# Performance work log

Measured on AMD Instinct MI355X. Metric: run time of the kernel, lower is better.

The kernel has to match this reference:

```python
import jax, jax.numpy as jnp
import numpy as np
from jax import lax

sg = lax.stop_gradient

# (kernel, stride, pad, pool_k, pool_s) for the 7 conv blocks
CFG = [(16, 2, 7, 8, 4), (12, 2, 5, 4, 2), (9, 1, 4, 5, 2), (7, 1, 3, 4, 2),
       (5, 1, 2, 2, 2), (3, 1, 1, 2, 2), (3, 1, 1, 2, 2)]
W_SHAPES = [(8, 1, 16), (12, 8, 12), (32, 12, 9), (64, 32, 7),
            (64, 64, 5), (64, 64, 3), (72, 64, 3)]
CH = [8, 12, 32, 64, 64, 64, 72]


def bin_act(x):
    # forward: sign(x); backward: clipped-quadratic surrogate (STE)
    s = jnp.sign(x)
    le = (x < -1.0).astype(x.dtype)
    ri = (x >= 1.0).astype(x.dtype)
    cl = ((x >= -1.0) & (x < 0.0)).astype(x.dtype)
    cr = ((x >= 0.0) & (x < 1.0)).astype(x.dtype)
    out = cl * (2.0 + x) * x + cr * (2.0 - x) * x + ri - le
    return sg(s) + out - sg(out)


def bin_wei(w, axes):
    # forward: scale * sign(w) with scale = mean|w| (detached); backward through tanh (STE)
    scale = sg(jnp.mean(jnp.abs(w), axis=axes, keepdims=True))
    t = jnp.tanh(w)
    return sg(scale * jnp.sign(w)) + t - sg(t)


def conv1d(x, w, stride, pad):
    return lax.conv_general_dilated(x, w, (stride,), [(pad, pad)],
                                    dimension_numbers=('NCH', 'OIH', 'NCH'))


def maxpool1d(x, k, s):
    return lax.reduce_window(x, -jnp.inf, lax.max, (1, 1, k), (1, 1, s), 'VALID')


def batchnorm1d(x, gamma, beta, eps=1e-5):
    # training-mode BN: batch statistics over (N, L), biased variance
    m = jnp.mean(x, axis=(0, 2), keepdims=True)
    v = jnp.mean((x - m) ** 2, axis=(0, 2), keepdims=True)
    return gamma[None, :, None] * (x - m) / jnp.sqrt(v + eps) + beta[None, :, None]


def _forward(x, ws, gs, bs, wfc):
    for w, g, b, (k, s, p, pk, ps) in zip(ws, gs, bs, CFG):
        x = conv1d(x, bin_wei(w, (1, 2)), s, p)
        x = maxpool1d(x, pk, ps)
        x = batchnorm1d(x, g, b)
        x = bin_act(x)
    x = x.reshape(x.shape[0], -1)                 # [B, 72*3]
    return x @ bin_wei(wfc, (1,)).T               # [B, classCount]


def setup_inputs() -> dict:
    key = jax.random.key(0)
    ks = jax.random.split(key, 9)
    inp = {'x': jax.random.normal(ks[0], (2048, 1, 3600), dtype=jnp.float32)}
    for i, shp in enumerate(W_SHAPES):
        inp[f'w{i+1}'] = jax.random.uniform(ks[i + 1], shp, dtype=jnp.float32) * 0.32
        inp[f'g{i+1}'] = jnp.ones((CH[i],), jnp.float32)
        inp[f'b{i+1}'] = jnp.zeros((CH[i],), jnp.float32)
    inp['wfc'] = jax.random.uniform(ks[8], (5, 216), dtype=jnp.float32) * 0.32
    return inp


def reference(x, w1, w2, w3, w4, w5, w6, w7,
              g1, g2, g3, g4, g5, g6, g7,
              b1, b2, b3, b4, b5, b6, b7, wfc):
    ws = [w1, w2, w3, w4, w5, w6, w7]
    gs = [g1, g2, g3, g4, g5, g6, g7]
    bs = [b1, b2, b3, b4, b5, b6, b7]
    return _forward(x, ws, gs, bs, wfc)
```

## Files before the change

kernel.cpp:

```cpp
#include <hip/hip_runtime.h>
#include <math.h>
#include <stdint.h>

#define NBATCH 2048
#define NSLOT 32

struct Args {
    const float* x;
    const float* W[7];
    const float* G[7];
    const float* Bt[7];
    const float* WFC;
    float* out;
    float* bufA;
    float* bufB;
    double* stats;
    float* wsc;
    uint32_t* wmb;
};

__device__ __forceinline__ float signf(float v) {
    return (v > 0.f) ? 1.f : ((v < 0.f) ? -1.f : 0.f);
}

__global__ __launch_bounds__(256) void k_setup(Args a) {
    const int blk = blockIdx.x, tid = threadIdx.x;
    for (int i = blk * 256 + tid; i < NSLOT * 632; i += 391 * 256) a.stats[i] = 0.0;

    if (blk < 321 && tid < 64) {
        const int cum[9] = {0,8,20,52,116,180,244,316,321};
        const int per[8] = {16,96,108,224,320,192,192,216};
        const float* wsrc[8] = {a.W[0],a.W[1],a.W[2],a.W[3],a.W[4],a.W[5],a.W[6],a.WFC};
        int o = blk, L = 0;
        while (L < 7 && o >= cum[L + 1]) ++L;
        const int oo = o - cum[L], p = per[L];
        const float* wo = wsrc[L] + (size_t)oo * p;
        float s = 0.f;
        for (int i = tid; i < p; i += 64) s += fabsf(wo[i]);
        #pragma unroll
        for (int off = 32; off; off >>= 1) s += __shfl_down(s, off);
        if (tid == 0) a.wsc[o] = s / (float)p;
    }

    const int gid = (blk - 384) * 256 + tid;
    if (blk >= 384 && blk <= 388 && gid >= 0 && gid < 1176) {
        const int cum[5]  = {0,448,768,960,1176};
        const int cin[4]  = {32,64,64,64};
        const int kk[4]   = {7,5,3,3};
        const int wpp[4]  = {1,2,2,2};
        const int woff[4] = {356,804,1444,1828};
        const float* wsrc[4] = {a.W[3],a.W[4],a.W[5],a.W[6]};
        int L = 0;
        while (L < 3 && gid >= cum[L + 1]) ++L;
        const int idx = gid - cum[L];
        const int K = kk[L], CIN = cin[L], WPP = wpp[L];
        const int o = idx / K, k = idx - o * K;
        const float* w = wsrc[L];
        uint32_t m0 = 0, m1 = 0;
        for (int c = 0; c < CIN; ++c) {
            const float v = w[((size_t)o * CIN + c) * K + k];
            const uint32_t bit = (v < 0.f) ? 1u : 0u;
            int bp = c;
            if (CIN == 64) bp = 16 * (c & 3) + (c >> 2);
            else if (CIN == 32) bp = 8 * (c & 3) + (c >> 2);
            if (bp < 32) m0 |= bit << bp; else m1 |= bit << (bp - 32);
        }
        uint32_t* dst = a.wmb + woff[L] + (size_t)idx * WPP;
        dst[0] = m0;
        if (WPP == 2) dst[1] = m1;
    }

    if (blk == 389 && tid < 12) {
        const float* w = a.W[1];
        const int o = tid;
        #pragma unroll
        for (int g = 0; g < 3; ++g) {
            uint32_t word = 0;
            #pragma unroll
            for (int j = 0; j < 4; ++j) {
                const int k = 4 * g + j;
                uint32_t by = 0;
                #pragma unroll
                for (int c = 0; c < 8; ++c)
                    by |= (w[((size_t)o * 8 + c) * 12 + k] < 0.f ? 1u : 0u) << c;
                word |= by << (8 * j);
            }
            a.wmb[o * 3 + g] = word;
        }
    }
    if (blk == 390 && tid < 64) {
        const float* w = a.W[2];
        const int o = tid >> 1, ph = tid & 1;
        uint32_t mk[9];
        #pragma unroll
        for (int k = 0; k < 9; ++k) {
            uint32_t m = 0;
            #pragma unroll
            for (int c = 0; c < 12; ++c)
                m |= (w[((size_t)o * 12 + c) * 9 + k] < 0.f ? 1u : 0u) << c;
            mk[k] = m;
        }
        uint32_t wd[5];
        if (ph == 0) { wd[0]=mk[0]|(mk[1]<<16); wd[1]=mk[2]|(mk[3]<<16);
                       wd[2]=mk[4]|(mk[5]<<16); wd[3]=mk[6]|(mk[7]<<16); wd[4]=mk[8]; }
        else         { wd[0]=mk[0]<<16; wd[1]=mk[1]|(mk[2]<<16);
                       wd[2]=mk[3]|(mk[4]<<16); wd[3]=mk[5]|(mk[6]<<16); wd[4]=mk[7]|(mk[8]<<16); }
        #pragma unroll
        for (int g = 0; g < 5; ++g) a.wmb[36 + o * 10 + ph * 5 + g] = wd[g];
    }
}

__global__ __launch_bounds__(256) void k_conv1(Args a) {
    __shared__ float wgs[128];
    __shared__ double sred[16];
    const int n = blockIdx.x, tid = threadIdx.x, l = tid & 63;
    if (tid < 128) wgs[tid] = signf(a.W[0][tid]);
    if (tid < 16)  sred[tid] = 0.0;
    __syncthreads();
    const int r = tid;
    const float* xn = a.x + (size_t)n * 3600;
    float m0[8], m1[8];
    #pragma unroll
    for (int ch = 0; ch < 8; ++ch) { m0[ch] = 0.f; m1[ch] = 0.f; }
    if (r < 225) {
        float f[40];
        const int g0 = 16 * r - 8;
        #pragma unroll
        for (int b = 0; b < 10; ++b) {
            const int gg = g0 + 4 * b;
            if (gg >= 0 && gg <= 3596) {
                const float4 v = *(const float4*)(xn + gg);
                f[4*b] = v.x; f[4*b+1] = v.y; f[4*b+2] = v.z; f[4*b+3] = v.w;
            } else {
                f[4*b] = 0.f; f[4*b+1] = 0.f; f[4*b+2] = 0.f; f[4*b+3] = 0.f;
            }
        }
        #pragma unroll
        for (int ch = 0; ch < 8; ++ch) {
            float acc[12];
            #pragma unroll
            for (int j = 0; j < 12; ++j) acc[j] = 0.f;
            #pragma unroll
            for (int k = 0; k < 16; ++k) {
                const float wk = wgs[ch * 16 + k];
                #pragma unroll
                for (int j = 0; j < 12; ++j)
                    acc[j] = fmaf(f[2*j + 1 + k], wk, acc[j]);
            }
            const float lo  = fmaxf(fmaxf(acc[0], acc[1]), fmaxf(acc[2], acc[3]));
            const float mid = fmaxf(fmaxf(acc[4], acc[5]), fmaxf(acc[6], acc[7]));
            const float hi  = fmaxf(fmaxf(acc[8], acc[9]), fmaxf(acc[10], acc[11]));
            const float sc = a.wsc[ch];
            m0[ch] = fmaxf(lo, mid) * sc;
            m1[ch] = (r < 224) ? fmaxf(mid, hi) * sc : 0.f;
        }
        float* on = a.bufA + ((size_t)n * 449 + 2 * r) * 8;
        *(float4*)(on + 0) = make_float4(m0[0], m0[1], m0[2], m0[3]);
        *(float4*)(on + 4) = make_float4(m0[4], m0[5], m0[6], m0[7]);
        if (r < 224) {
            *(float4*)(on + 8)  = make_float4(m1[0], m1[1], m1[2], m1[3]);
            *(float4*)(on + 12) = make_float4(m1[4], m1[5], m1[6], m1[7]);
        }
    }
    #pragma unroll
    for (int ch = 0; ch < 8; ++ch) {
        double sS = (double)m0[ch] + (double)m1[ch];
        double s2 = (double)m0[ch] * m0[ch] + (double)m1[ch] * m1[ch];
        #pragma unroll
        for (int off = 32; off; off >>= 1) {
            sS += __shfl_down(sS, off);
            s2 += __shfl_down(s2, off);
        }
        if (l == 0) {
            atomicAdd(&sred[ch], sS);
            atomicAdd(&sred[8 + ch], s2);
        }
    }
    __syncthreads();
    if (tid < 16) {
        double* so = a.stats + (size_t)(n & (NSLOT - 1)) * 16;
        atomicAdd(&so[tid], sred[tid]);
    }
}

template <int CIN, int LIN, int O, int K, int STRIDE, int PAD,
          int PK, int PS, int LP, int WPP, int LPB, int NS, bool SF64>
__device__ __forceinline__ void bin_body(
    const float* __restrict__ xprev, const uint32_t* __restrict__ wm,
    const float* __restrict__ wsc, const float* __restrict__ wsc_prev,
    const double* __restrict__ stats_in,
    const float* __restrict__ gamma, const float* __restrict__ beta,
    const double cntInv, float* __restrict__ out, double* __restrict__ stats_out)
{
    constexpr int OL    = (O < 64) ? O : 64;
    constexpr int PO    = 64 / OL;
    constexpr int WPW   = 4 / NS;
    constexpr int SPAN  = (PK - 1) * STRIDE + K;
    constexpr int QLEN  = WPW * LPB * PS * STRIDE + SPAN;
    constexpr int XM64A =
        (WPP == 2)   ? (QLEN + 3)
      : (CIN == 8)   ? ((QLEN + 48) + 7) / 8
      : (CIN == 12)  ? ((2 * (QLEN + 10)) + 7) / 8
      : ((QLEN + 5) / 2 + 2);
    constexpr int F     = 2 * CIN;
    constexpr int FW    = (F > 64) ? 128 : 64;
    constexpr int XBASE = (CIN == 8 || CIN == 12) ? 0
                        : (WPP == 1) ? -(PAD & 1) : 0;

    __shared__ uint64_t xmbuf[NS][XM64A];
    __shared__ long long foldU[4][FW];
    __shared__ int sS[4][O], sS2[4][O];

    const int tid  = threadIdx.x;
    const int wv   = tid >> 6;
    const int l    = tid & 63;
    const int sloc = wv / WPW;
    const int wvs  = wv % WPW;
    uint64_t* xm64 = xmbuf[sloc];
    uint32_t* xm32 = (uint32_t*)xm64;
    uint16_t* xm16 = (uint16_t*)xm64;
    uint8_t*  xm8  = (uint8_t*)xm64;

    const int n   = blockIdx.x * NS + sloc;
    const int lp0 = wvs * LPB;
    const int lp1 = (lp0 + LPB < LP) ? lp0 + LPB : LP;

    const float* xn = xprev + (size_t)n * LIN * CIN;

    {
        const long long* stI = (const long long*)stats_in;
        long long pa = 0, pb_ = 0;
        double da = 0.0;
        #pragma unroll
        for (int s8 = 0; s8 < 8; ++s8) {
            const int s = (wv << 3) + s8;
            if constexpr (SF64) {
                if (l < F) da += stats_in[s * F + l];
            } else {
                if (l < ((F < 64) ? F : 64)) pa += stI[s * F + l];
                if constexpr (F > 64) { if (l < F - 64) pb_ += stI[s * F + 64 + l]; }
            }
        }
        if constexpr (SF64) foldU[wv][l] = __double_as_longlong(da);
        else {
            foldU[wv][l] = pa;
            if constexpr (F > 64) foldU[wv][64 + l] = pb_;
        }
    }
    __syncthreads();
    float aA = 0.f, aB = 0.f;
    {
        double t0 = 0.0, t1 = 0.0;
        if constexpr (SF64) {
            double tot = 0.0;
            #pragma unroll
            for (int w = 0; w < 4; ++w) tot += __longlong_as_double(foldU[w][l]);
            t0 = tot;
            t1 = __shfl(tot, CIN + l);
        } else if constexpr (F > 64) {
            long long a0 = 0, a1 = 0;
            #pragma unroll
            for (int w = 0; w < 4; ++w) { a0 += foldU[w][l]; a1 += foldU[w][64 + l]; }
            t0 = (double)a0; t1 = (double)a1;
        } else {
            long long a0 = 0;
            #pragma unroll
            for (int w = 0; w < 4; ++w) a0 += foldU[w][l];
            const double tot = (double)a0;
            t0 = tot;
            t1 = __shfl(tot, CIN + l);
        }
        if (l < CIN) {
            double mean, E2;
            if constexpr (SF64) { mean = t0 * cntInv; E2 = t1 * cntInv; }
            else {
                const double w = (double)wsc_prev[l];
                mean = w * t0 * cntInv; E2 = w * w * t1 * cntInv;
            }
            const double var = E2 - mean * mean;
            const double inv = 1.0 / sqrt(var + 1e-5);
            const double av  = (double)gamma[l] * inv;
            aA = (float)av;
            aB = (float)((double)beta[l] - mean * av);
        }
    }

    if constexpr (CIN == 64) {
        constexpr int STP = WPW * 4;
        constexpr int MAXIT = (LIN + STP - 1) / STP;
        const int sub = l & 15, grp = l >> 4;
        const float a0 = __shfl(aA, 4*sub),     b0 = __shfl(aB, 4*sub);
        const float a1 = __shfl(aA, 4*sub + 1), b1 = __shfl(aB, 4*sub + 1);
        const float a2 = __shfl(aA, 4*sub + 2), b2 = __shfl(aB, 4*sub + 2);
        const float a3 = __shfl(aA, 4*sub + 3), b3 = __shfl(aB, 4*sub + 3);
        #pragma unroll
        for (int it = 0; it < MAXIT; ++it) {
            const int pb = wvs * 4 + it * STP;
            const int pos = pb + grp;
            const bool valid = pos < LIN;
            const float4 v = *(const float4*)(xn + (size_t)(valid ? pos : 0) * 64 + 4*sub);
            const unsigned long long bal0 = __ballot(valid && (fmaf(a0, v.x, b0) < 0.f));
            const unsigned long long bal1 = __ballot(valid && (fmaf(a1, v.y, b1) < 0.f));
            const unsigned long long bal2 = __ballot(valid && (fmaf(a2, v.z, b2) < 0.f));
            const unsigned long long bal3 = __ballot(valid && (fmaf(a3, v.w, b3) < 0.f));
            if (l < 4 && pb + l < LIN) {
                const uint64_t m = ((bal0 >> (16*l)) & 0xFFFFull)
                                 | (((bal1 >> (16*l)) & 0xFFFFull) << 16)
                                 | (((bal2 >> (16*l)) & 0xFFFFull) << 32)
                                 | (((bal3 >> (16*l)) & 0xFFFFull) << 48);
                xm64[pb + l - XBASE] = m;
            }
        }
    } else if constexpr (CIN == 32) {
        constexpr int STP = WPW * 8;
        constexpr int MAXIT = (LIN + STP - 1) / STP;
        const int sub = l & 7, grp = l >> 3;
        const float a0 = __shfl(aA, 4*sub),     b0 = __shfl(aB, 4*sub);
        const float a1 = __shfl(aA, 4*sub + 1), b1 = __shfl(aB, 4*sub + 1);
        const float a2 = __shfl(aA, 4*sub + 2), b2 = __shfl(aB, 4*sub + 2);
        const float a3 = __shfl(aA, 4*sub + 3), b3 = __shfl(aB, 4*sub + 3);
        #pragma unroll
        for (int it = 0; it < MAXIT; ++it) {
            const int pb = wvs * 8 + it * STP;
            const int pos = pb + grp;
            const bool valid = pos < LIN;
            const float4 v = *(const float4*)(xn + (size_t)(valid ? pos : 0) * 32 + 4*sub);
            const unsigned long long bal0 = __ballot(valid && (fmaf(a0, v.x, b0) < 0.f));
            const unsigned long long bal1 = __ballot(valid && (fmaf(a1, v.y, b1) < 0.f));
            const unsigned long long bal2 = __ballot(valid && (fmaf(a2, v.z, b2) < 0.f));
            const unsigned long long bal3 = __ballot(valid && (fmaf(a3, v.w, b3) < 0.f));
            if (l < 8 && pb + l < LIN) {
                const uint32_t m = (uint32_t)((bal0 >> (8*l)) & 0xFFull)
                                 | ((uint32_t)((bal1 >> (8*l)) & 0xFFull) << 8)
                                 | ((uint32_t)((bal2 >> (8*l)) & 0xFFull) << 16)
                                 | ((uint32_t)((bal3 >> (8*l)) & 0xFFull) << 24);
                xm32[pb + l - XBASE] = m;
            }
        }
    } else if constexpr (CIN == 8) {
        constexpr int STP = WPW * 32;
        constexpr int MAXIT = (LIN + STP - 1) / STP;
        const int sub = l & 1, grp = l >> 1;
        const float a0 = __shfl(aA, 4*sub),     b0 = __shfl(aB, 4*sub);
        const float a1 = __shfl(aA, 4*sub + 1), b1 = __shfl(aB, 4*sub + 1);
        const float a2 = __shfl(aA, 4*sub + 2), b2 = __shfl(aB, 4*sub + 2);
        const float a3 = __shfl(aA, 4*sub + 3), b3 = __shfl(aB, 4*sub + 3);
        #pragma unroll
        for (int it = 0; it < MAXIT; ++it) {
            const int pb = wvs * 32 + it * STP;
            const int pos = pb + grp;
            const bool valid = pos < LIN;
            const float4 v = *(const float4*)(xn + (size_t)(valid ? pos : 0) * 8 + 4*sub);
            const unsigned long long bal0 = __ballot(valid && (fmaf(a0, v.x, b0) < 0.f));
            const unsigned long long bal1 = __ballot(valid && (fmaf(a1, v.y, b1) < 0.f));
            const unsigned long long bal2 = __ballot(valid && (fmaf(a2, v.z, b2) < 0.f));
            const unsigned long long bal3 = __ballot(valid && (fmaf(a3, v.w, b3) < 0.f));
            if (l < 32 && pb + l < LIN) {
                const uint32_t t0 = (uint32_t)((bal0 >> (2*l)) & 3ull);
                const uint32_t t1 = (uint32_t)((bal1 >> (2*l)) & 3ull);
                const uint32_t t2 = (uint32_t)((bal2 >> (2*l)) & 3ull);
                const uint32_t t3 = (uint32_t)((bal3 >> (2*l)) & 3ull);
                const uint32_t m = (t0 & 1) | ((t1 & 1) << 1) | ((t2 & 1) << 2) | ((t3 & 1) << 3)
                                 | ((t0 >> 1) << 4) | ((t1 >> 1) << 5) | ((t2 >> 1) << 6) | ((t3 >> 1) << 7);
                xm8[pb + l - XBASE] = (uint8_t)m;
            }
        }
    } else {
        constexpr int PPW = 64 / CIN;
        constexpr int STP = WPW * PPW;
        constexpr int MAXIT = (LIN + STP - 1) / STP;
        const int pw = l / CIN, c = l - pw * CIN;
        const float myA = __shfl(aA, c), myB = __shfl(aB, c);
        const bool lact = (pw < PPW);
        #pragma unroll
        for (int it = 0; it < MAXIT; ++it) {
            const int pb = wvs * PPW + it * STP;
            const int pos = pb + pw;
            const bool act = lact && (pos < LIN) && (pb < LIN);
            float v = 0.f;
            if (act) v = fmaf(myA, xn[(size_t)pb * CIN + l], myB);
            const unsigned long long bal = __ballot(act && (v < 0.f));
            if (act && c == 0) {
                const uint32_t mk = (uint32_t)((bal >> (pw * CIN)) & ((1u << CIN) - 1));
                xm16[pos - XBASE] = (uint16_t)mk;
            }
        }
    }
    __syncthreads();

    float* on = out + (size_t)n * LP * O;

    if constexpr (WPP == 2) {
        const uint64_t* wmp = (const uint64_t*)wm;
        uint64_t wr[K];
        #pragma unroll
        for (int k = 0; k < K; ++k) wr[k] = wmp[l * K + k];
        uint64_t wr2[K];
        const int oo2 = 64 + ((O > 64 && l < O - 64) ? l : 0);
        if constexpr (O > 64) {
            #pragma unroll
            for (int k = 0; k < K; ++k) wr2[k] = wmp[oo2 * K + k];
        }
        const float myws  = wsc[l];
        const float myws2 = (O > 64 && l < O - 64) ? wsc[64 + l] : 0.f;
        int accS = 0, accS2 = 0, accSb = 0, accS2b = 0;

        #pragma unroll
        for (int li = 0; li < LPB; ++li) {
            const int lp = lp0 + li;
            if (lp < lp1) {
                const int lo = lp * PS * STRIDE - PAD;
                int m = -1000000, m2 = -1000000;
                if (lo >= 0 && lo + SPAN <= LIN) {
                    uint64_t tw[SPAN];
                    #pragma unroll
                    for (int t = 0; t < SPAN; ++t) tw[t] = xm64[lo - XBASE + t];
                    #pragma unroll
                    for (int j = 0; j < PK; ++j) {
                        int p = 0;
                        #pragma unroll
                        for (int k = 0; k < K; ++k)
                            p += __popcll(tw[j * STRIDE + k] ^ wr[k]);
                        m = max(m, CIN * K - 2 * p);
                        if constexpr (O > 64) {
                            int p2 = 0;
                            #pragma unroll
                            for (int k = 0; k < K; ++k)
                                p2 += __popcll(tw[j * STRIDE + k] ^ wr2[k]);
                            m2 = max(m2, CIN * K - 2 * p2);
                        }
                    }
                } else {
                    #pragma unroll
                    for (int j = 0; j < PK; ++j) {
                        const int base = lo + j * STRIDE;
                        int p = 0, nv = 0, p2 = 0;
                        #pragma unroll
                        for (int k = 0; k < K; ++k) {
                            const int q = base + k;
                            if (q >= 0 && q < LIN) {
                                ++nv;
                                const uint64_t xv = xm64[q - XBASE];
                                p += __popcll(xv ^ wr[k]);
                                if constexpr (O > 64) p2 += __popcll(xv ^ wr2[k]);
                            }
                        }
                        m = max(m, CIN * nv - 2 * p);
                        if constexpr (O > 64) m2 = max(m2, CIN * nv - 2 * p2);
                    }
                }
                on[lp * O + l] = (float)m * myws;
                accS += m; accS2 += m * m;
                if constexpr (O > 64) {
                    if (l < O - 64) {
                        on[lp * O + 64 + l] = (float)m2 * myws2;
                        accSb += m2; accS2b += m2 * m2;
                    }
                }
            }
        }
        sS[wv][l] = accS; sS2[wv][l] = accS2;
        if constexpr (O > 64) {
            if (l < O - 64) { sS[wv][64 + l] = accSb; sS2[wv][64 + l] = accS2b; }
        }
    } else if constexpr (CIN == 8) {
        const int po = l / OL, oo = l - po * OL;
        const bool cact = (po < PO);
        const float myws = cact ? wsc[oo] : 0.f;
        const int osel = cact ? oo : 0;
        const uint32_t wr0 = wm[osel*3], wr1 = wm[osel*3+1], wr2 = wm[osel*3+2];
        uint32_t wb[12];
        #pragma unroll
        for (int k = 0; k < 12; ++k)
            wb[k] = ((k < 4 ? wr0 : (k < 8 ? wr1 : wr2)) >> (8 * (k & 3))) & 255u;
        const uint32_t* xw = (const uint32_t*)xm64;
        int accS = 0, accS2 = 0;

        #pragma unroll 2
        for (int lp = lp0 + po; lp < lp1; lp += PO) {
            const int lo = lp * PS * STRIDE - PAD;
            int m = -1000000;
            if (lo >= 0 && lo + SPAN <= LIN) {
                const int bb = lo - XBASE;
                const int w0 = bb >> 2;
                uint32_t tw[6];
                #pragma unroll
                for (int i = 0; i < 6; ++i) tw[i] = xw[w0 + i];
                #pragma unroll
                for (int j = 0; j < PK; ++j) {
                    const int wo = (j + 1) >> 1;
                    uint32_t e0, e1, e2;
                    if (j & 1) {
                        e0 = (tw[wo]   >> 8) | (tw[wo+1] << 24);
                        e1 = (tw[wo+1] >> 8) | (tw[wo+2] << 24);
                        e2 = (tw[wo+2] >> 8) | (tw[wo+3] << 24);
                    } else {
                        e0 = (tw[wo]   >> 24) | (tw[wo+1] << 8);
                        e1 = (tw[wo+1] >> 24) | (tw[wo+2] << 8);
                        e2 = (tw[wo+2] >> 24) | (tw[wo+3] << 8);
                    }
                    const int p = __popc(e0 ^ wr0) + __popc(e1 ^ wr1) + __popc(e2 ^ wr2);
                    m = max(m, 96 - 2 * p);
                }
            } else {
                #pragma unroll
                for (int j = 0; j < PK; ++j) {
                    const int base = lo + j * STRIDE;
                    int p = 0, nv = 0;
                    #pragma unroll
                    for (int k = 0; k < 12; ++k) {
                        const int q = base + k;
                        if (q >= 0 && q < LIN) { ++nv; p += __popc((uint32_t)xm8[q - XBASE] ^ wb[k]); }
                    }
                    m = max(m, 8 * nv - 2 * p);
                }
            }
            if (cact) {
                on[lp * O + oo] = (float)m * myws;
                accS += m; accS2 += m * m;
            }
        }
        int t = accS, t2 = accS2;
        #pragma unroll
        for (int g = 1; g < PO; ++g) {
            t  += __shfl(accS,  l + g * OL);
            t2 += __shfl(accS2, l + g * OL);
        }
        if (l < OL) { sS[wv][l] = t; sS2[wv][l] = t2; }
        else if (l < O) { sS[wv][l] = 0; sS2[wv][l] = 0; }
    } else if constexpr (CIN == 12) {
        const int po = l / OL, oo = l - po * OL;
        const bool cact = (po < PO);
        const float myws = cact ? wsc[oo] : 0.f;
        const int osel = cact ? oo : 0;
        uint32_t wE[5], wO[5];
        #pragma unroll
        for (int g = 0; g < 5; ++g) { wE[g] = wm[osel*10 + g]; wO[g] = wm[osel*10 + 5 + g]; }
        uint32_t we16[9];
        we16[0]=wE[0]&0xFFFFu; we16[1]=wE[0]>>16; we16[2]=wE[1]&0xFFFFu; we16[3]=wE[1]>>16;
        we16[4]=wE[2]&0xFFFFu; we16[5]=wE[2]>>16; we16[6]=wE[3]&0xFFFFu; we16[7]=wE[3]>>16;
        we16[8]=wE[4]&0xFFFFu;
        const uint32_t* xw = (const uint32_t*)xm64;
        int accS = 0, accS2 = 0;

        #pragma unroll 2
        for (int lp = lp0 + po; lp < lp1; lp += PO) {
            const int lo = lp * PS * STRIDE - PAD;
            int m = -1000000;
            if (lo >= 0 && lo + SPAN <= LIN) {
                const int s0 = (lo - XBASE) >> 1;
                uint32_t tw[7];
                #pragma unroll
                for (int i = 0; i < 7; ++i) tw[i] = xw[s0 + i];
                #pragma unroll
                for (int j = 0; j < PK; ++j) {
                    const int o_ = j >> 1;
                    int p;
                    if (j & 1)
                        p = __popc((tw[o_] & 0xFFFF0000u) ^ wO[0]) + __popc(tw[o_+1] ^ wO[1])
                          + __popc(tw[o_+2] ^ wO[2]) + __popc(tw[o_+3] ^ wO[3])
                          + __popc(tw[o_+4] ^ wO[4]);
                    else
                        p = __popc(tw[o_] ^ wE[0]) + __popc(tw[o_+1] ^ wE[1])
                          + __popc(tw[o_+2] ^ wE[2]) + __popc(tw[o_+3] ^ wE[3])
                          + __popc((tw[o_+4] & 0xFFFFu) ^ wE[4]);
                    m = max(m, 108 - 2 * p);
                }
            } else {
                #pragma unroll
                for (int j = 0; j < PK; ++j) {
                    const int base = lo + j * STRIDE;
                    int p = 0, nv = 0;
                    #pragma unroll
                    for (int k = 0; k < 9; ++k) {
                        const int q = base + k;
                        if (q >= 0 && q < LIN) { ++nv; p += __popc((uint32_t)xm16[q - XBASE] ^ we16[k]); }
                    }
                    m = max(m, 12 * nv - 2 * p);
                }
            }
            if (cact) {
                on[lp * O + oo] = (float)m * myws;
                accS += m; accS2 += m * m;
            }
        }
        int t = accS, t2 = accS2;
        #pragma unroll
        for (int g = 1; g < PO; ++g) {
            t  += __shfl(accS,  l + g * OL);
            t2 += __shfl(accS2, l + g * OL);
        }
        if (l < OL) { sS[wv][l] = t; sS2[wv][l] = t2; }
    } else {
        const int po = l / OL, oo = l - po * OL;
        const bool cact = (po < PO);
        const float myws = cact ? wsc[oo] : 0.f;
        uint32_t wr[K];
        #pragma unroll
        for (int k = 0; k < K; ++k) wr[k] = wm[(cact ? oo : 0) * K + k];
        int accS = 0, accS2 = 0;

        constexpr int PAIRS = (SPAN + 1) / 2;
        #pragma unroll 2
        for (int lp = lp0 + po; lp < lp1; lp += PO) {
            const int lo = lp * PS * STRIDE - PAD;
            int m = -1000000;
            if (lo >= 0 && lo + SPAN <= LIN) {
                uint32_t tw[PAIRS * 2];
                const int e0 = (lo - XBASE) >> 1;
                #pragma unroll
                for (int i = 0; i < PAIRS; ++i) {
                    const uint64_t u64v = xm64[e0 + i];
                    tw[2 * i]     = (uint32_t)u64v;
                    tw[2 * i + 1] = (uint32_t)(u64v >> 32);
                }
                #pragma unroll
                for (int j = 0; j < PK; ++j) {
                    int p = 0;
                    #pragma unroll
                    for (int k = 0; k < K; ++k)
                        p += __popc(tw[j * STRIDE + k] ^ wr[k]);
                    m = max(m, CIN * K - 2 * p);
                }
            } else {
                #pragma unroll
                for (int j = 0; j < PK; ++j) {
                    const int base = lo + j * STRIDE;
                    int p = 0, nv = 0;
                    #pragma unroll
                    for (int k = 0; k < K; ++k) {
                        const int q = base + k;
                        if (q >= 0 && q < LIN) { ++nv; p += __popc(xm32[q - XBASE] ^ wr[k]); }
                    }
                    m = max(m, CIN * nv - 2 * p);
                }
            }
            if (cact) {
                on[lp * O + oo] = (float)m * myws;
                accS += m; accS2 += m * m;
            }
        }
        int t = accS, t2 = accS2;
        #pragma unroll
        for (int g = 1; g < PO; ++g) {
            t  += __shfl(accS,  l + g * OL);
            t2 += __shfl(accS2, l + g * OL);
        }
        if (l < OL) { sS[wv][l] = t; sS2[wv][l] = t2; }
    }
    __syncthreads();

    const int slot = ((NS == 1) ? n : (int)blockIdx.x) & (NSLOT - 1);
    unsigned long long* soU =
        (unsigned long long*)stats_out + (size_t)slot * 2 * O;
    for (int t = tid; t < 2 * O; t += 256) {
        int tot;
        if (t < O) tot = sS[0][t] + sS[1][t] + sS[2][t] + sS[3][t];
        else { const int f = t - O; tot = sS2[0][f] + sS2[1][f] + sS2[2][f] + sS2[3][f]; }
        atomicAdd(&soU[t], (unsigned long long)(long long)tot);
    }
}

#define BIN_PARAMS \
    const float* __restrict__ xprev, const uint32_t* __restrict__ wm, \
    const float* __restrict__ wsc, const float* __restrict__ wsc_prev, \
    const double* __restrict__ stats_in, \
    const float* __restrict__ gamma, const float* __restrict__ beta, \
    const double cntInv, float* __restrict__ out, double* __restrict__ stats_out
#define BIN_ARGS xprev, wm, wsc, wsc_prev, stats_in, gamma, beta, cntInv, out, stats_out

__global__ __launch_bounds__(256) void k_bin2(BIN_PARAMS) { bin_body< 8,449,12,12,2,5,4,2,111,1,28,1,true >(BIN_ARGS); }
__global__ __launch_bounds__(256) void k_bin3(BIN_PARAMS) { bin_body<12,111,32, 9,1,4,5,2, 54,1,14,1,false>(BIN_ARGS); }
__global__ __launch_bounds__(256) void k_bin4(BIN_PARAMS) { bin_body<32, 54,64, 7,1,3,4,2, 26,1, 7,1,false>(BIN_ARGS); }
__global__ __launch_bounds__(256) void k_bin5(BIN_PARAMS) { bin_body<64, 26,64, 5,1,2,2,2, 13,2, 7,2,false>(BIN_ARGS); }
__global__ __launch_bounds__(256) void k_bin6(BIN_PARAMS) { bin_body<64, 13,64, 3,1,1,2,2,  6,2, 3,2,false>(BIN_ARGS); }
__global__ __launch_bounds__(256) void k_bin7(BIN_PARAMS) { bin_body<64,  6,72, 3,1,1,2,2,  3,2, 2,2,false>(BIN_ARGS); }

__global__ __launch_bounds__(256) void k_fc(Args a) {
    const int n = blockIdx.x * 4 + (int)(threadIdx.x >> 6);
    const int l = (int)(threadIdx.x & 63);
    const long long* st = (const long long*)(a.stats + 15616);
    long long s = 0, s2 = 0, sb = 0, s2b = 0;
    #pragma unroll 4
    for (int sl = 0; sl < NSLOT; ++sl) {
        s  += st[sl * 144 + l];
        s2 += st[sl * 144 + 72 + l];
        if (l < 8) {
            sb  += st[sl * 144 + 64 + l];
            s2b += st[sl * 144 + 72 + 64 + l];
        }
    }
    float aA0, aB0, aA1 = 0.f, aB1 = 0.f;
    {
        const double w = (double)a.wsc[244 + l];
        const double mean = w * (double)s / 6144.0;
        const double E2   = w * w * (double)s2 / 6144.0;
        const double var  = E2 - mean * mean;
        const double inv  = 1.0 / sqrt(var + 1e-5);
        const double aa   = (double)a.G[6][l] * inv;
        aA0 = (float)aa; aB0 = (float)((double)a.Bt[6][l] - mean * aa);
    }
    if (l < 8) {
        const double w = (double)a.wsc[244 + 64 + l];
        const double mean = w * (double)sb / 6144.0;
        const double E2   = w * w * (double)s2b / 6144.0;
        const double var  = E2 - mean * mean;
        const double inv  = 1.0 / sqrt(var + 1e-5);
        const double aa   = (double)a.G[6][64 + l] * inv;
        aA1 = (float)aa; aB1 = (float)((double)a.Bt[6][64 + l] - mean * aa);
    }
    const float* p7 = a.bufA + (size_t)n * 216;
    float acc[5] = {0.f, 0.f, 0.f, 0.f, 0.f};
    #pragma unroll
    for (int j = 0; j < 4; ++j) {
        const int i = l + 64 * j;
        const int ic = (i < 216) ? i : 215;
        const int c = ic / 3, lp = ic - 3 * c;
        float aa = __shfl(aA0, c);
        float bb = __shfl(aB0, c);
        const float aaH = __shfl(aA1, c - 64);
        const float bbH = __shfl(aB1, c - 64);
        if (c >= 64) { aa = aaH; bb = bbH; }
        if (i < 216) {
            const float av = signf(fmaf(aa, p7[lp * 72 + c], bb));
            #pragma unroll
            for (int o = 0; o < 5; ++o)
                acc[o] += av * signf(a.WFC[o * 216 + i]);
        }
    }
    #pragma unroll
    for (int o = 0; o < 5; ++o) {
        float v = acc[o];
        #pragma unroll
        for (int off = 32; off; off >>= 1) v += __shfl_down(v, off);
        if (l == 0) a.out[(size_t)n * 5 + o] = v * a.wsc[316 + o];
    }
}

extern "C" void kernel_launch(void* const* d_in, const int* in_sizes, int n_in,
                              void* d_out, int out_size, void* d_ws, size_t ws_size,
                              hipStream_t stream) {
    Args a;
    a.x = (const float*)d_in[0];
    for (int i = 0; i < 7; ++i) {
        a.W[i]  = (const float*)d_in[1 + 3 * i];
        a.G[i]  = (const float*)d_in[2 + 3 * i];
        a.Bt[i] = (const float*)d_in[3 + 3 * i];
    }
    a.WFC = (const float*)d_in[22];
    a.out = (float*)d_out;

    char* ws = (char*)d_ws;
    a.bufA  = (float*)ws;
    a.bufB  = (float*)(ws + 29425664);
    a.stats = (double*)(ws + 43057152);
    a.wsc   = (float*)(ws + 43218944);
    a.wmb   = (uint32_t*)d_out;

    k_setup<<<391, 256, 0, stream>>>(a);
    k_conv1<<<NBATCH, 256, 0, stream>>>(a);
    k_bin2<<<dim3(NBATCH, 1), 256, 0, stream>>>(
        a.bufA, a.wmb + 0, a.wsc + 8, a.wsc, a.stats + 0, a.G[0], a.Bt[0],
        1.0/919552.0, a.bufB, a.stats + 512);
    k_bin3<<<dim3(NBATCH, 1), 256, 0, stream>>>(
        a.bufB, a.wmb + 36, a.wsc + 20, a.wsc + 8, a.stats + 512, a.G[1], a.Bt[1],
        1.0/227328.0, a.bufA, a.stats + 1280);
    k_bin4<<<dim3(NBATCH, 1), 256, 0, stream>>>(
        a.bufA, a.wmb + 356, a.wsc + 52, a.wsc + 20, a.stats + 1280, a.G[2], a.Bt[2],
        1.0/110592.0, a.bufB, a.stats + 3328);
    k_bin5<<<dim3(NBATCH / 2, 1), 256, 0, stream>>>(
        a.bufB, a.wmb + 804, a.wsc + 116, a.wsc + 52, a.stats + 3328, a.G[3], a.Bt[3],
        1.0/53248.0, a.bufA, a.stats + 7424);
    k_bin6<<<dim3(NBATCH / 2, 1), 256, 0, stream>>>(
        a.bufA, a.wmb + 1444, a.wsc + 180, a.wsc + 116, a.stats + 7424, a.G[4], a.Bt[4],
        1.0/26624.0, a.bufB, a.stats + 11520);
    k_bin7<<<dim3(NBATCH / 2, 1), 256, 0, stream>>>(
        a.bufB, a.wmb + 1828, a.wsc + 244, a.wsc + 180, a.stats + 11520, a.G[5], a.Bt[5],
        1.0/12288.0, a.bufA, a.stats + 15616);
    k_fc<<<NBATCH / 4, 256, 0, stream>>>(a);
}
```

Before: 246.8 us.

## Store intermediate conv-pool outputs as offset integer codes in uint8/uint16

Inter-layer activations were float maxpooled binary-conv results times the weight scale. They are now stored as raw integer counts plus a per-layer offset, in uint8 or uint16, and the consumer reapplies the previous layer's weight scale on load. This cuts global memory write and read traffic between the layer kernels by two to four times. It relies on the integer range fitting the chosen offsets and widths, and adds a little conversion arithmetic on load.

```diff
diff --git a/kernel.cpp b/kernel.cpp
--- a/kernel.cpp
+++ b/kernel.cpp
@@ -184,13 +184,14 @@
 }
 
 template <int CIN, int LIN, int O, int K, int STRIDE, int PAD,
-          int PK, int PS, int LP, int WPP, int LPB, int NS, bool SF64>
+          int PK, int PS, int LP, int WPP, int LPB, int NS, bool SF64,
+          int IOFF, int OOFF>
 __device__ __forceinline__ void bin_body(
-    const float* __restrict__ xprev, const uint32_t* __restrict__ wm,
+    const void* __restrict__ xprev, const uint32_t* __restrict__ wm,
     const float* __restrict__ wsc, const float* __restrict__ wsc_prev,
     const double* __restrict__ stats_in,
     const float* __restrict__ gamma, const float* __restrict__ beta,
-    const double cntInv, float* __restrict__ out, double* __restrict__ stats_out)
+    const double cntInv, void* __restrict__ out, double* __restrict__ stats_out)
 {
     constexpr int OL    = (O < 64) ? O : 64;
     constexpr int PO    = 64 / OL;
@@ -225,7 +226,7 @@
     const int lp0 = wvs * LPB;
     const int lp1 = (lp0 + LPB < LP) ? lp0 + LPB : LP;
 
-    const float* xn = xprev + (size_t)n * LIN * CIN;
+    const float wpv = (l < CIN) ? wsc_prev[l] : 0.f;
 
     {
         const long long* stI = (const long long*)stats_in;
@@ -274,7 +275,7 @@
             double mean, E2;
             if constexpr (SF64) { mean = t0 * cntInv; E2 = t1 * cntInv; }
             else {
-                const double w = (double)wsc_prev[l];
+                const double w = (double)wpv;
                 mean = w * t0 * cntInv; E2 = w * w * t1 * cntInv;
             }
             const double var = E2 - mean * mean;
@@ -286,6 +287,7 @@
     }
 
     if constexpr (CIN == 64) {
+        const uint16_t* xp = (const uint16_t*)xprev + (size_t)n * LIN * 64;
         constexpr int STP = WPW * 4;
         constexpr int MAXIT = (LIN + STP - 1) / STP;
         const int sub = l & 15, grp = l >> 4;
@@ -293,16 +295,22 @@
         const float a1 = __shfl(aA, 4*sub + 1), b1 = __shfl(aB, 4*sub + 1);
         const float a2 = __shfl(aA, 4*sub + 2), b2 = __shfl(aB, 4*sub + 2);
         const float a3 = __shfl(aA, 4*sub + 3), b3 = __shfl(aB, 4*sub + 3);
+        const float p0 = __shfl(wpv, 4*sub),     p1 = __shfl(wpv, 4*sub + 1);
+        const float p2 = __shfl(wpv, 4*sub + 2), p3 = __shfl(wpv, 4*sub + 3);
         #pragma unroll
         for (int it = 0; it < MAXIT; ++it) {
             const int pb = wvs * 4 + it * STP;
             const int pos = pb + grp;
             const bool valid = pos < LIN;
-            const float4 v = *(const float4*)(xn + (size_t)(valid ? pos : 0) * 64 + 4*sub);
-            const unsigned long long bal0 = __ballot(valid && (fmaf(a0, v.x, b0) < 0.f));
-            const unsigned long long bal1 = __ballot(valid && (fmaf(a1, v.y, b1) < 0.f));
-            const unsigned long long bal2 = __ballot(valid && (fmaf(a2, v.z, b2) < 0.f));
-            const unsigned long long bal3 = __ballot(valid && (fmaf(a3, v.w, b3) < 0.f));
+            const ushort4 s = *(const ushort4*)(xp + (size_t)(valid ? pos : 0) * 64 + 4*sub);
+            const float v0 = (float)((int)s.x - IOFF) * p0;
+            const float v1 = (float)((int)s.y - IOFF) * p1;
+            const float v2 = (float)((int)s.z - IOFF) * p2;
+            const float v3 = (float)((int)s.w - IOFF) * p3;
+            const unsigned long long bal0 = __ballot(valid && (fmaf(a0, v0, b0) < 0.f));
+            const unsigned long long bal1 = __ballot(valid && (fmaf(a1, v1, b1) < 0.f));
+            const unsigned long long bal2 = __ballot(valid && (fmaf(a2, v2, b2) < 0.f));
+            const unsigned long long bal3 = __ballot(valid && (fmaf(a3, v3, b3) < 0.f));
             if (l < 4 && pb + l < LIN) {
                 const uint64_t m = ((bal0 >> (16*l)) & 0xFFFFull)
                                  | (((bal1 >> (16*l)) & 0xFFFFull) << 16)
@@ -312,6 +320,7 @@
             }
         }
     } else if constexpr (CIN == 32) {
+        const uint8_t* xp = (const uint8_t*)xprev + (size_t)n * LIN * 32;
         constexpr int STP = WPW * 8;
         constexpr int MAXIT = (LIN + STP - 1) / STP;
         const int sub = l & 7, grp = l >> 3;
@@ -319,16 +328,22 @@
         const float a1 = __shfl(aA, 4*sub + 1), b1 = __shfl(aB, 4*sub + 1);
         const float a2 = __shfl(aA, 4*sub + 2), b2 = __shfl(aB, 4*sub + 2);
         const float a3 = __shfl(aA, 4*sub + 3), b3 = __shfl(aB, 4*sub + 3);
+        const float p0 = __shfl(wpv, 4*sub),     p1 = __shfl(wpv, 4*sub + 1);
+        const float p2 = __shfl(wpv, 4*sub + 2), p3 = __shfl(wpv, 4*sub + 3);
         #pragma unroll
         for (int it = 0; it < MAXIT; ++it) {
             const int pb = wvs * 8 + it * STP;
             const int pos = pb + grp;
             const bool valid = pos < LIN;
-            const float4 v = *(const float4*)(xn + (size_t)(valid ? pos : 0) * 32 + 4*sub);
-            const unsigned long long bal0 = __ballot(valid && (fmaf(a0, v.x, b0) < 0.f));
-            const unsigned long long bal1 = __ballot(valid && (fmaf(a1, v.y, b1) < 0.f));
-            const unsigned long long bal2 = __ballot(valid && (fmaf(a2, v.z, b2) < 0.f));
-            const unsigned long long bal3 = __ballot(valid && (fmaf(a3, v.w, b3) < 0.f));
+            const uchar4 s = *(const uchar4*)(xp + (size_t)(valid ? pos : 0) * 32 + 4*sub);
+            const float v0 = (float)((int)s.x - IOFF) * p0;
+            const float v1 = (float)((int)s.y - IOFF) * p1;
+            const float v2 = (float)((int)s.z - IOFF) * p2;
+            const float v3 = (float)((int)s.w - IOFF) * p3;
+            const unsigned long long bal0 = __ballot(valid && (fmaf(a0, v0, b0) < 0.f));
+            const unsigned long long bal1 = __ballot(valid && (fmaf(a1, v1, b1) < 0.f));
+            const unsigned long long bal2 = __ballot(valid && (fmaf(a2, v2, b2) < 0.f));
+            const unsigned long long bal3 = __ballot(valid && (fmaf(a3, v3, b3) < 0.f));
             if (l < 8 && pb + l < LIN) {
                 const uint32_t m = (uint32_t)((bal0 >> (8*l)) & 0xFFull)
                                  | ((uint32_t)((bal1 >> (8*l)) & 0xFFull) << 8)
@@ -338,6 +353,7 @@
             }
         }
     } else if constexpr (CIN == 8) {
+        const float* xn = (const float*)xprev + (size_t)n * LIN * 8;
         constexpr int STP = WPW * 32;
         constexpr int MAXIT = (LIN + STP - 1) / STP;
         const int sub = l & 1, grp = l >> 1;
@@ -366,11 +382,13 @@
             }
         }
     } else {
+        const uint8_t* xp = (const uint8_t*)xprev + (size_t)n * LIN * 12;
         constexpr int PPW = 64 / CIN;
         constexpr int STP = WPW * PPW;
         constexpr int MAXIT = (LIN + STP - 1) / STP;
         const int pw = l / CIN, c = l - pw * CIN;
         const float myA = __shfl(aA, c), myB = __shfl(aB, c);
+        const float myP = __shfl(wpv, c);
         const bool lact = (pw < PPW);
         #pragma unroll
         for (int it = 0; it < MAXIT; ++it) {
@@ -378,7 +396,7 @@
             const int pos = pb + pw;
             const bool act = lact && (pos < LIN) && (pb < LIN);
             float v = 0.f;
-            if (act) v = fmaf(myA, xn[(size_t)pb * CIN + l], myB);
+            if (act) v = fmaf(myA, (float)((int)xp[(size_t)pb * 12 + l] - IOFF) * myP, myB);
             const unsigned long long bal = __ballot(act && (v < 0.f));
             if (act && c == 0) {
                 const uint32_t mk = (uint32_t)((bal >> (pw * CIN)) & ((1u << CIN) - 1));
@@ -388,9 +406,8 @@
     }
     __syncthreads();
 
-    float* on = out + (size_t)n * LP * O;
-
     if constexpr (WPP == 2) {
+        uint16_t* on16 = (uint16_t*)out + (size_t)n * LP * O;
         const uint64_t* wmp = (const uint64_t*)wm;
         uint64_t wr[K];
         #pragma unroll
@@ -401,8 +418,6 @@
             #pragma unroll
             for (int k = 0; k < K; ++k) wr2[k] = wmp[oo2 * K + k];
         }
-        const float myws  = wsc[l];
-        const float myws2 = (O > 64 && l < O - 64) ? wsc[64 + l] : 0.f;
         int accS = 0, accS2 = 0, accSb = 0, accS2b = 0;
 
         #pragma unroll
@@ -449,11 +464,11 @@
                         if constexpr (O > 64) m2 = max(m2, CIN * nv - 2 * p2);
                     }
                 }
-                on[lp * O + l] = (float)m * myws;
+                on16[lp * O + l] = (uint16_t)(m + OOFF);
                 accS += m; accS2 += m * m;
                 if constexpr (O > 64) {
                     if (l < O - 64) {
-                        on[lp * O + 64 + l] = (float)m2 * myws2;
+                        on16[lp * O + 64 + l] = (uint16_t)(m2 + OOFF);
                         accSb += m2; accS2b += m2 * m2;
                     }
                 }
@@ -464,9 +479,9 @@
             if (l < O - 64) { sS[wv][64 + l] = accSb; sS2[wv][64 + l] = accS2b; }
         }
     } else if constexpr (CIN == 8) {
+        uint8_t* on8 = (uint8_t*)out + (size_t)n * LP * O;
         const int po = l / OL, oo = l - po * OL;
         const bool cact = (po < PO);
-        const float myws = cact ? wsc[oo] : 0.f;
         const int osel = cact ? oo : 0;
         const uint32_t wr0 = wm[osel*3], wr1 = wm[osel*3+1], wr2 = wm[osel*3+2];
         uint32_t wb[12];
@@ -516,7 +531,7 @@
                 }
             }
             if (cact) {
-                on[lp * O + oo] = (float)m * myws;
+                on8[lp * O + oo] = (uint8_t)(m + OOFF);
                 accS += m; accS2 += m * m;
             }
         }
@@ -529,9 +544,9 @@
         if (l < OL) { sS[wv][l] = t; sS2[wv][l] = t2; }
         else if (l < O) { sS[wv][l] = 0; sS2[wv][l] = 0; }
     } else if constexpr (CIN == 12) {
+        uint8_t* on8 = (uint8_t*)out + (size_t)n * LP * O;
         const int po = l / OL, oo = l - po * OL;
         const bool cact = (po < PO);
-        const float myws = cact ? wsc[oo] : 0.f;
         const int osel = cact ? oo : 0;
         uint32_t wE[5], wO[5];
         #pragma unroll
@@ -580,7 +595,7 @@
                 }
             }
             if (cact) {
-                on[lp * O + oo] = (float)m * myws;
+                on8[lp * O + oo] = (uint8_t)(m + OOFF);
                 accS += m; accS2 += m * m;
             }
         }
@@ -592,9 +607,9 @@
         }
         if (l < OL) { sS[wv][l] = t; sS2[wv][l] = t2; }
     } else {
+        uint16_t* on16 = (uint16_t*)out + (size_t)n * LP * O;
         const int po = l / OL, oo = l - po * OL;
         const bool cact = (po < PO);
-        const float myws = cact ? wsc[oo] : 0.f;
         uint32_t wr[K];
         #pragma unroll
         for (int k = 0; k < K; ++k) wr[k] = wm[(cact ? oo : 0) * K + k];
@@ -636,7 +651,7 @@
                 }
             }
             if (cact) {
-                on[lp * O + oo] = (float)m * myws;
+                on16[lp * O + oo] = (uint16_t)(m + OOFF);
                 accS += m; accS2 += m * m;
             }
         }
@@ -662,19 +677,19 @@
 }
 
 #define BIN_PARAMS \
-    const float* __restrict__ xprev, const uint32_t* __restrict__ wm, \
+    const void* __restrict__ xprev, const uint32_t* __restrict__ wm, \
     const float* __restrict__ wsc, const float* __restrict__ wsc_prev, \
     const double* __restrict__ stats_in, \
     const float* __restrict__ gamma, const float* __restrict__ beta, \
-    const double cntInv, float* __restrict__ out, double* __restrict__ stats_out
+    const double cntInv, void* __restrict__ out, double* __restrict__ stats_out
 #define BIN_ARGS xprev, wm, wsc, wsc_prev, stats_in, gamma, beta, cntInv, out, stats_out
 
-__global__ __launch_bounds__(256) void k_bin2(BIN_PARAMS) { bin_body< 8,449,12,12,2,5,4,2,111,1,28,1,true >(BIN_ARGS); }
-__global__ __launch_bounds__(256) void k_bin3(BIN_PARAMS) { bin_body<12,111,32, 9,1,4,5,2, 54,1,14,1,false>(BIN_ARGS); }
-__global__ __launch_bounds__(256) void k_bin4(BIN_PARAMS) { bin_body<32, 54,64, 7,1,3,4,2, 26,1, 7,1,false>(BIN_ARGS); }
-__global__ __launch_bounds__(256) void k_bin5(BIN_PARAMS) { bin_body<64, 26,64, 5,1,2,2,2, 13,2, 7,2,false>(BIN_ARGS); }
-__global__ __launch_bounds__(256) void k_bin6(BIN_PARAMS) { bin_body<64, 13,64, 3,1,1,2,2,  6,2, 3,2,false>(BIN_ARGS); }
-__global__ __launch_bounds__(256) void k_bin7(BIN_PARAMS) { bin_body<64,  6,72, 3,1,1,2,2,  3,2, 2,2,false>(BIN_ARGS); }
+__global__ __launch_bounds__(256) void k_bin2(BIN_PARAMS) { bin_body< 8,449,12,12,2,5,4,2,111,1,28,1,true ,  0, 96>(BIN_ARGS); }
+__global__ __launch_bounds__(256) void k_bin3(BIN_PARAMS) { bin_body<12,111,32, 9,1,4,5,2, 54,1,14,1,false, 96,108>(BIN_ARGS); }
+__global__ __launch_bounds__(256) void k_bin4(BIN_PARAMS) { bin_body<32, 54,64, 7,1,3,4,2, 26,1, 7,1,false,108,224>(BIN_ARGS); }
+__global__ __launch_bounds__(256) void k_bin5(BIN_PARAMS) { bin_body<64, 26,64, 5,1,2,2,2, 13,2, 7,2,false,224,320>(BIN_ARGS); }
+__global__ __launch_bounds__(256) void k_bin6(BIN_PARAMS) { bin_body<64, 13,64, 3,1,1,2,2,  6,2, 3,2,false,320,192>(BIN_ARGS); }
+__global__ __launch_bounds__(256) void k_bin7(BIN_PARAMS) { bin_body<64,  6,72, 3,1,1,2,2,  3,2, 2,2,false,192,192>(BIN_ARGS); }
 
 __global__ __launch_bounds__(256) void k_fc(Args a) {
     const int n = blockIdx.x * 4 + (int)(threadIdx.x >> 6);
@@ -690,9 +705,11 @@
             s2b += st[sl * 144 + 72 + 64 + l];
         }
     }
+    const float w7  = a.wsc[244 + l];
+    const float w7b = (l < 8) ? a.wsc[244 + 64 + l] : 0.f;
     float aA0, aB0, aA1 = 0.f, aB1 = 0.f;
     {
-        const double w = (double)a.wsc[244 + l];
+        const double w = (double)w7;
         const double mean = w * (double)s / 6144.0;
         const double E2   = w * w * (double)s2 / 6144.0;
         const double var  = E2 - mean * mean;
@@ -701,7 +718,7 @@
         aA0 = (float)aa; aB0 = (float)((double)a.Bt[6][l] - mean * aa);
     }
     if (l < 8) {
-        const double w = (double)a.wsc[244 + 64 + l];
+        const double w = (double)w7b;
         const double mean = w * (double)sb / 6144.0;
         const double E2   = w * w * (double)s2b / 6144.0;
         const double var  = E2 - mean * mean;
@@ -709,7 +726,7 @@
         const double aa   = (double)a.G[6][64 + l] * inv;
         aA1 = (float)aa; aB1 = (float)((double)a.Bt[6][64 + l] - mean * aa);
     }
-    const float* p7 = a.bufA + (size_t)n * 216;
+    const uint16_t* p7 = (const uint16_t*)a.bufA + (size_t)n * 216;
     float acc[5] = {0.f, 0.f, 0.f, 0.f, 0.f};
     #pragma unroll
     for (int j = 0; j < 4; ++j) {
@@ -718,11 +735,14 @@
         const int c = ic / 3, lp = ic - 3 * c;
         float aa = __shfl(aA0, c);
         float bb = __shfl(aB0, c);
+        float ww = __shfl(w7, c);
         const float aaH = __shfl(aA1, c - 64);
         const float bbH = __shfl(aB1, c - 64);
-        if (c >= 64) { aa = aaH; bb = bbH; }
+        const float wwH = __shfl(w7b, c - 64);
+        if (c >= 64) { aa = aaH; bb = bbH; ww = wwH; }
         if (i < 216) {
-            const float av = signf(fmaf(aa, p7[lp * 72 + c], bb));
+            const float v = (float)((int)p7[lp * 72 + c] - 192) * ww;
+            const float av = signf(fmaf(aa, v, bb));
             #pragma unroll
             for (int o = 0; o < 5; ++o)
                 acc[o] += av * signf(a.WFC[o * 216 + i]);
```

Result: no change. 246.8 us (-0.0%).
